# Kernel tuning notes

Measured on AMD Instinct MI355X. Metric: run time of the kernel, lower is better.

## Reference

```python
import jax, jax.numpy as jnp
import numpy as np

B, T, C = 2, 2048, 1024
NUM_HEADS, QK_LEN, V_LEN = 16, 64, 64


def setup_inputs() -> dict:
    key = jax.random.key(0)
    ks = jax.random.split(key, 11)
    s = 0.02
    return {
        "Q": jax.random.normal(ks[0], (B, T, C), jnp.float32),
        "K": jax.random.normal(ks[1], (B, T, C), jnp.float32),
        "V": jax.random.normal(ks[2], (B, T, C), jnp.float32),
        # Linear weights stored as (in, out); y = x @ W + b
        "Wq": jax.random.normal(ks[3], (C, NUM_HEADS * QK_LEN), jnp.float32) * s,
        "bq": jnp.zeros((NUM_HEADS * QK_LEN,), jnp.float32),
        "Wk": jax.random.normal(ks[4], (C, NUM_HEADS * QK_LEN), jnp.float32) * s,
        "bk": jnp.zeros((NUM_HEADS * QK_LEN,), jnp.float32),
        "Wv": jax.random.normal(ks[5], (C, NUM_HEADS * V_LEN), jnp.float32) * s,
        "bv": jnp.zeros((NUM_HEADS * V_LEN,), jnp.float32),
        "Wo": jax.random.normal(ks[6], (NUM_HEADS * V_LEN, C), jnp.float32) * s,
        "bo": jnp.zeros((C,), jnp.float32),
    }


def _split_heads(x, n_heads, d):
    b, t, _ = x.shape
    return x.reshape(b, t, n_heads, d).transpose(0, 2, 1, 3)  # (B,H,T,d)


def reference(Q, K, V, Wq, bq, Wk, bk, Wv, bv, Wo, bo):
    q = _split_heads(Q @ Wq + bq, NUM_HEADS, QK_LEN)   # (B,H,T,dk)
    k = _split_heads(K @ Wk + bk, NUM_HEADS, QK_LEN)   # (B,H,T,dk)
    v = _split_heads(V @ Wv + bv, NUM_HEADS, V_LEN)    # (B,H,T,dv)

    scale = 1.0 / jnp.sqrt(jnp.asarray(QK_LEN, q.dtype))
    scores = jnp.einsum("bhqd,bhkd->bhqk", q, k) * scale  # (B,H,T,T)
    attn = jax.nn.softmax(scores, axis=-1)
    out = jnp.einsum("bhqk,bhkd->bhqd", attn, v)           # (B,H,T,dv)

    out = out.transpose(0, 2, 1, 3).reshape(Q.shape[0], Q.shape[1], NUM_HEADS * V_LEN)
    return out @ Wo + bo
```

## Files before the change

### kernel.cpp

```cpp
#include <hip/hip_runtime.h>
#include <hip/hip_bf16.h>
#include <math.h>

constexpr int B = 2, T = 2048, C = 1024, H = 16, D = 64;
constexpr int M = B * T;
constexpr float SCALE_L2E = 0.125f * 1.4426950408889634f;

typedef __attribute__((ext_vector_type(8))) short s16x8;
typedef __attribute__((ext_vector_type(4))) short s16x4;
typedef __attribute__((ext_vector_type(4))) float fv4;

typedef unsigned short ushort_t;

static __device__ __forceinline__ ushort_t f2bf(float x) {
    union { float f; unsigned u; } c; c.f = x;
    unsigned u = c.u + 0x7FFFu + ((c.u >> 16) & 1u);
    return (ushort_t)(u >> 16);
}

static __device__ __forceinline__ int cvt_pk_bf16(float lo, float hi) {
    int r;
    asm("v_cvt_pk_bf16_f32 %0, %1, %2" : "=v"(r) : "v"(lo), "v"(hi));
    return r;
}

#define GLDS(gp, lp) __builtin_amdgcn_global_load_lds( \
    (const __attribute__((address_space(1))) void*)(gp), \
    (__attribute__((address_space(3))) void*)(lp), 16, 0, 0)

__global__ __launch_bounds__(256) void prep(
    const float* __restrict__ W0, const float* __restrict__ W1,
    const float* __restrict__ W2, const float* __restrict__ W3,
    ushort_t* __restrict__ Wt)
{
    __shared__ ushort_t tile[64][72];
    const int tid = threadIdx.x;
    const int idx = blockIdx.x;
    const int s = idx >> 8;
    const float* W = (s == 0) ? W0 : (s == 1) ? W1 : (s == 2) ? W2 : W3;
    const int k0 = (idx & 15) * 64, n0 = ((idx >> 4) & 15) * 64;
#pragma unroll
    for (int it = 0; it < 4; it++) {
        int f = it * 256 + tid;
        int r = f >> 4, c4 = (f & 15) * 4;
        float4 x = *(const float4*)(W + (size_t)(k0 + r) * C + n0 + c4);
        *(int*)&tile[r][c4]     = cvt_pk_bf16(x.x, x.y);
        *(int*)&tile[r][c4 + 2] = cvt_pk_bf16(x.z, x.w);
    }
    __syncthreads();
#pragma unroll
    for (int it = 0; it < 4; it++) {
        int f = it * 256 + tid;
        int rr = f >> 4, c4 = (f & 15) * 4;
        union { s16x4 v; ushort_t u[4]; } u;
#pragma unroll
        for (int j = 0; j < 4; j++) u.u[j] = tile[c4 + j][rr];
        *(s16x4*)(Wt + (size_t)(s * 1024 + n0 + rr) * 1024 + k0 + c4) = u.v;
    }
}

__global__ __launch_bounds__(256) void gemm_qkv(
    const float* __restrict__ Qf, const float* __restrict__ Kf,
    const float* __restrict__ Vf, const ushort_t* __restrict__ Wt,
    const float* __restrict__ bq, const float* __restrict__ bk,
    const float* __restrict__ bv,
    ushort_t* __restrict__ qw, ushort_t* __restrict__ kw,
    ushort_t* __restrict__ vt)
{
    __shared__ ushort_t sm[17408];
    ushort_t* As0 = sm;
    ushort_t* Bs0 = sm + 8192;

    const int tid = threadIdx.x;
    const int w = tid >> 6, lane = tid & 63;
    const int quad = lane >> 4, lc = lane & 15;
    const int wm = w & 1, wn = w >> 1;

    const int lin = blockIdx.y * 24 + blockIdx.x;
    const int xcd = lin % 8;
    const int i_ = lin / 8;
    const int s = i_ >> 5;
    const int r_ = i_ & 31;
    const int m0 = (xcd * 4 + (r_ >> 3)) * 128;
    const int nt = s * 8 + (r_ & 7);
    const int nsec0 = (nt & 7) * 128;

    const float* Af = (s == 0) ? Qf : (s == 1) ? Kf : Vf;
    const ushort_t* Btbase = Wt + (size_t)nt * 128 * 1024;

    const int srow = (w << 4) + (lane >> 2);
    const int ske  = (lane & 3) * 8;

    const int ar = tid >> 1;
    const int ah = (tid & 1) * 16;
    const float* apb = Af + (size_t)(m0 + ar) * 1024 + ah;

    fv4 acc[4][4] = {};

    auto stageB = [&](int k0, int buf) {
#pragma unroll
        for (int i = 0; i < 2; i++) {
            int row = i * 64 + srow;
            GLDS(Btbase + (size_t)row * 1024 + k0 + ske,
                 Bs0 + buf * 4096 + i * 2048 + w * 512);
        }
    };
    float4 areg[4];
    auto loadA = [&](int k0) {
        const float4* p = (const float4*)(apb + k0);
        areg[0] = p[0]; areg[1] = p[1]; areg[2] = p[2]; areg[3] = p[3];
    };
    auto writeA = [&](int buf) {
        union { s16x8 v; int i[4]; } u0, u1;
        u0.i[0] = cvt_pk_bf16(areg[0].x, areg[0].y);
        u0.i[1] = cvt_pk_bf16(areg[0].z, areg[0].w);
        u0.i[2] = cvt_pk_bf16(areg[1].x, areg[1].y);
        u0.i[3] = cvt_pk_bf16(areg[1].z, areg[1].w);
        u1.i[0] = cvt_pk_bf16(areg[2].x, areg[2].y);
        u1.i[1] = cvt_pk_bf16(areg[2].z, areg[2].w);
        u1.i[2] = cvt_pk_bf16(areg[3].x, areg[3].y);
        u1.i[3] = cvt_pk_bf16(areg[3].z, areg[3].w);
        ushort_t* dst = As0 + buf * 4096 + ar * 32 + ah;
        *(s16x8*)dst = u0.v;
        *(s16x8*)(dst + 8) = u1.v;
    };

    stageB(0, 0);
    loadA(0);
    writeA(0);
    __syncthreads();

    for (int k0 = 0; k0 < 1024; k0 += 32) {
        const int cur = (k0 >> 5) & 1;
        const bool pf = (k0 + 32 < 1024);
        if (pf) { stageB(k0 + 32, cur ^ 1); loadA(k0 + 32); }

        s16x8 af[4], bf[4];
#pragma unroll
        for (int ms = 0; ms < 4; ms++)
            af[ms] = *(const s16x8*)(As0 + cur * 4096 + (wm * 64 + ms * 16 + lc) * 32 + quad * 8);
#pragma unroll
        for (int ns = 0; ns < 4; ns++)
            bf[ns] = *(const s16x8*)(Bs0 + cur * 4096 + (wn * 64 + ns * 16 + lc) * 32 + quad * 8);
#pragma unroll
        for (int ms = 0; ms < 4; ms++)
#pragma unroll
            for (int ns = 0; ns < 4; ns++)
                acc[ms][ns] = __builtin_amdgcn_mfma_f32_16x16x32_bf16(
                    af[ms], bf[ns], acc[ms][ns], 0, 0, 0);

        if (pf) writeA(cur ^ 1);
        __syncthreads();
    }

    if (s == 2) {
        ushort_t* tp = sm;
#pragma unroll
        for (int ns = 0; ns < 4; ns++) {
            const int nl = wn * 64 + ns * 16 + lc;
            const float bias = bv[nsec0 + nl];
#pragma unroll
            for (int ms = 0; ms < 4; ms++) {
                const int ml = wm * 64 + ms * 16 + quad * 4;
                union { s16x4 v; int i2[2]; } u;
                u.i2[0] = cvt_pk_bf16(acc[ms][ns][0] + bias, acc[ms][ns][1] + bias);
                u.i2[1] = cvt_pk_bf16(acc[ms][ns][2] + bias, acc[ms][ns][3] + bias);
                *(s16x4*)&tp[nl * 136 + ml] = u.v;
            }
        }
        __syncthreads();
        const int b_ = m0 >> 11, t0 = m0 & 2047;
#pragma unroll
        for (int it = 0; it < 8; it++) {
            const int row = it * 16 + (tid >> 4);
            const int ch = tid & 15;
            const int n = nsec0 + row;
            const int h_ = n >> 6, d_ = n & 63;
            s16x8 v8 = *(const s16x8*)&tp[row * 136 + ch * 8];
            *(s16x8*)(vt + ((size_t)(b_ * H + h_) * 64 + d_) * T + t0 + ch * 8) = v8;
        }
        return;
    }

    const float* biasp = (s == 0) ? bq : bk;
    const float premul = (s == 0) ? SCALE_L2E : 1.0f;
    ushort_t* outp = (s == 0) ? qw : kw;

#pragma unroll
    for (int ns = 0; ns < 4; ns++) {
        const int nl = nsec0 + wn * 64 + ns * 16 + lc;
        const float bias = biasp[nl];
        const int h_ = nl >> 6, d_ = nl & 63;
#pragma unroll
        for (int ms = 0; ms < 4; ms++) {
#pragma unroll
            for (int r = 0; r < 4; r++) {
                int m = m0 + wm * 64 + ms * 16 + quad * 4 + r;
                float val = (acc[ms][ns][r] + bias) * premul;
                int b_ = m >> 11, t_ = m & (T - 1);
                size_t bh = (size_t)(b_ * H + h_);
                outp[((bh * T + t_) << 6) + d_] = f2bf(val);
            }
        }
    }
}

__global__ __launch_bounds__(256) void gemm_final(
    const ushort_t* __restrict__ A, const ushort_t* __restrict__ Wot,
    const float* __restrict__ bo, float* __restrict__ out)
{
    __shared__ ushort_t As[2][128 * 32];
    __shared__ ushort_t Bs[2][64 * 32];

    const int tid = threadIdx.x;
    const int w = tid >> 6, lane = tid & 63;
    const int quad = lane >> 4, lc = lane & 15;
    const int wm = w & 1, wn = w >> 1;

    const int lin = blockIdx.y * 16 + blockIdx.x;
    const int xcd = lin & 7;
    const int i_ = lin >> 3;
    const int m0 = (xcd * 4 + (i_ >> 4)) * 128;
    const int n0 = (i_ & 15) * 64;

    const int srow = (w << 4) + (lane >> 2);
    const int ske  = (lane & 3) * 8;

    fv4 acc[4][2] = {};

    auto stage = [&](int k0, int buf) {
        GLDS(A + (size_t)(m0 + srow) * 1024 + k0 + ske,      As[buf] + w * 512);
        GLDS(A + (size_t)(m0 + 64 + srow) * 1024 + k0 + ske, As[buf] + 2048 + w * 512);
        GLDS(Wot + (size_t)(n0 + srow) * 1024 + k0 + ske,    Bs[buf] + w * 512);
    };

    stage(0, 0);
    __syncthreads();

    for (int k0 = 0; k0 < 1024; k0 += 32) {
        const int cur = (k0 >> 5) & 1;
        if (k0 + 32 < 1024) stage(k0 + 32, cur ^ 1);

        s16x8 af[4], bf[2];
#pragma unroll
        for (int ms = 0; ms < 4; ms++)
            af[ms] = *(const s16x8*)(As[cur] + (wm * 64 + ms * 16 + lc) * 32 + quad * 8);
#pragma unroll
        for (int ns = 0; ns < 2; ns++)
            bf[ns] = *(const s16x8*)(Bs[cur] + (wn * 32 + ns * 16 + lc) * 32 + quad * 8);
#pragma unroll
        for (int ms = 0; ms < 4; ms++)
#pragma unroll
            for (int ns = 0; ns < 2; ns++)
                acc[ms][ns] = __builtin_amdgcn_mfma_f32_16x16x32_bf16(
                    af[ms], bf[ns], acc[ms][ns], 0, 0, 0);
        __syncthreads();
    }

#pragma unroll
    for (int ns = 0; ns < 2; ns++) {
        const int n = n0 + wn * 32 + ns * 16 + lc;
        const float bias = bo[n];
#pragma unroll
        for (int ms = 0; ms < 4; ms++) {
#pragma unroll
            for (int r = 0; r < 4; r++) {
                int m = m0 + wm * 64 + ms * 16 + quad * 4 + r;
                out[(size_t)m * 1024 + n] = acc[ms][ns][r] + bias;
            }
        }
    }
}

__global__ __launch_bounds__(256, 4) void attn(
    const ushort_t* __restrict__ q, const ushort_t* __restrict__ k,
    const ushort_t* __restrict__ vT, ushort_t* __restrict__ o)
{
    __shared__ alignas(16) ushort_t ks[2][64 * 64];
    __shared__ alignas(16) ushort_t vs[2][64 * 64];

    const int tid = threadIdx.x;
    const int w = tid >> 6, lane = tid & 63;
    const int quad = lane >> 4, lc = lane & 15;
    const int cs = lc & 7;
    const int qsub = w & 1, ksub = w >> 1;

    const int id = blockIdx.y * 32 + blockIdx.x;
    const int qt = (id >> 3) & 31;
    const int bh = (id & 7) * 4 + (id >> 8);

    s16x8 aq[2][2];
    const ushort_t* qb = q + ((size_t)bh * T + qt * 64 + qsub * 32) * D;
#pragma unroll
    for (int j = 0; j < 2; j++)
#pragma unroll
        for (int h = 0; h < 2; h++)
            aq[j][h] = *(const s16x8*)(qb + (size_t)(j * 16 + lc) * D + h * 32 + quad * 8);

    fv4 accO[2][4] = {};
    float psum[2] = {0.f, 0.f};

    const ushort_t* kb0 = k + (size_t)bh * T * D;
    const ushort_t* vb0 = vT + (size_t)bh * D * T;

    const int sr8 = lane >> 3;
    const int sch = (lane & 7) ^ sr8;

    auto stage = [&](int kt, int buf) {
#pragma unroll
        for (int i = 0; i < 2; i++) {
            const int r = w * 16 + i * 8 + sr8;
            GLDS(kb0 + (size_t)(kt * 64 + r) * 64 + sch * 8,
                 ks[buf] + (w * 16 + i * 8) * 64);
            GLDS(vb0 + (size_t)r * T + kt * 64 + sch * 8,
                 vs[buf] + (w * 16 + i * 8) * 64);
        }
    };

    stage(0, 0);
    __syncthreads();

    for (int kt = 0; kt < T / 64; kt++) {
        const int cur = kt & 1;
        if (kt + 1 < T / 64) stage(kt + 1, cur ^ 1);

        fv4 accST[2][2] = {};
        __builtin_amdgcn_s_setprio(1);
#pragma unroll
        for (int t4k = 0; t4k < 2; t4k++) {
            const int row = ksub * 32 + t4k * 16 + lc;
            s16x8 ak0 = *(const s16x8*)(ks[cur] + row * 64 + ((quad ^ cs) << 3));
            s16x8 ak1 = *(const s16x8*)(ks[cur] + row * 64 + (((quad + 4) ^ cs) << 3));
#pragma unroll
            for (int j = 0; j < 2; j++) {
                accST[j][t4k] = __builtin_amdgcn_mfma_f32_16x16x32_bf16(
                    ak0, aq[j][0], accST[j][t4k], 0, 0, 0);
                accST[j][t4k] = __builtin_amdgcn_mfma_f32_16x16x32_bf16(
                    ak1, aq[j][1], accST[j][t4k], 0, 0, 0);
            }
        }
        __builtin_amdgcn_s_setprio(0);

        s16x8 av[4];
#pragma unroll
        for (int t4v = 0; t4v < 4; t4v++) {
            const int row = t4v * 16 + lc;
            av[t4v] = *(const s16x8*)(vs[cur] + row * 64 + (((ksub * 4 + quad) ^ cs) << 3));
        }

#pragma unroll
        for (int j = 0; j < 2; j++) {
            float p0 = __builtin_amdgcn_exp2f(accST[j][0][0]);
            float p1 = __builtin_amdgcn_exp2f(accST[j][0][1]);
            float p2 = __builtin_amdgcn_exp2f(accST[j][0][2]);
            float p3 = __builtin_amdgcn_exp2f(accST[j][0][3]);
            float p4 = __builtin_amdgcn_exp2f(accST[j][1][0]);
            float p5 = __builtin_amdgcn_exp2f(accST[j][1][1]);
            float p6 = __builtin_amdgcn_exp2f(accST[j][1][2]);
            float p7 = __builtin_amdgcn_exp2f(accST[j][1][3]);
            psum[j] += ((p0 + p1) + (p2 + p3)) + ((p4 + p5) + (p6 + p7));

            int W00 = cvt_pk_bf16(p0, p1);
            int W01 = cvt_pk_bf16(p2, p3);
            int W10 = cvt_pk_bf16(p4, p5);
            int W11 = cvt_pk_bf16(p6, p7);
            asm("v_permlane32_swap_b32 %0, %1" : "+v"(W00), "+v"(W10));
            asm("v_permlane16_swap_b32 %0, %1" : "+v"(W00), "+v"(W10));
            asm("v_permlane32_swap_b32 %0, %1" : "+v"(W01), "+v"(W11));
            asm("v_permlane16_swap_b32 %0, %1" : "+v"(W01), "+v"(W11));

            union { int i[4]; s16x8 v; } pbu;
            pbu.i[0] = W00; pbu.i[1] = W01; pbu.i[2] = W10; pbu.i[3] = W11;

            __builtin_amdgcn_s_setprio(1);
#pragma unroll
            for (int t4v = 0; t4v < 4; t4v++)
                accO[j][t4v] = __builtin_amdgcn_mfma_f32_16x16x32_bf16(
                    av[t4v], pbu.v, accO[j][t4v], 0, 0, 0);
            __builtin_amdgcn_s_setprio(0);
        }

        __syncthreads();
    }

#pragma unroll
    for (int j = 0; j < 2; j++) {
        psum[j] += __shfl_xor(psum[j], 16);
        psum[j] += __shfl_xor(psum[j], 32);
    }

    float* sc = (float*)&ks[0][0];
#pragma unroll
    for (int c = 0; c < 4; c++) {
        const int j = c >> 1, tv = (c & 1) * 2;
        __syncthreads();
        if (ksub == 1) {
            *(fv4*)(sc + ((qsub * 64 + lane) * 8))     = accO[j][tv];
            *(fv4*)(sc + ((qsub * 64 + lane) * 8 + 4)) = accO[j][tv + 1];
        }
        __syncthreads();
        if (ksub == 0) {
            accO[j][tv]     += *(fv4*)(sc + ((qsub * 64 + lane) * 8));
            accO[j][tv + 1] += *(fv4*)(sc + ((qsub * 64 + lane) * 8 + 4));
        }
    }
    __syncthreads();
    if (ksub == 1) {
        sc[(qsub * 64 + lane) * 2]     = psum[0];
        sc[(qsub * 64 + lane) * 2 + 1] = psum[1];
    }
    __syncthreads();
    if (ksub == 0) {
        psum[0] += sc[(qsub * 64 + lane) * 2];
        psum[1] += sc[(qsub * 64 + lane) * 2 + 1];

        const int b_ = bh >> 4, h_ = bh & 15;
#pragma unroll
        for (int j = 0; j < 2; j++) {
            float inv = 1.0f / psum[j];
            int row = qt * 64 + qsub * 32 + j * 16 + lc;
            ushort_t* op = o + ((size_t)b_ * T + row) * C + h_ * 64;
#pragma unroll
            for (int t4v = 0; t4v < 4; t4v++) {
                union { s16x4 v; int i[2]; } u;
                u.i[0] = cvt_pk_bf16(accO[j][t4v][0] * inv, accO[j][t4v][1] * inv);
                u.i[1] = cvt_pk_bf16(accO[j][t4v][2] * inv, accO[j][t4v][3] * inv);
                *(s16x4*)(op + t4v * 16 + quad * 4) = u.v;
            }
        }
    }
}

extern "C" void kernel_launch(void* const* d_in, const int* in_sizes, int n_in,
                              void* d_out, int out_size, void* d_ws, size_t ws_size,
                              hipStream_t stream)
{
    const float* Q  = (const float*)d_in[0];
    const float* K  = (const float*)d_in[1];
    const float* V  = (const float*)d_in[2];
    const float* Wq = (const float*)d_in[3];
    const float* bq = (const float*)d_in[4];
    const float* Wk = (const float*)d_in[5];
    const float* bk = (const float*)d_in[6];
    const float* Wv = (const float*)d_in[7];
    const float* bv = (const float*)d_in[8];
    const float* Wo = (const float*)d_in[9];
    const float* bo = (const float*)d_in[10];
    float* out = (float*)d_out;

    ushort_t* ow = (ushort_t*)d_ws;
    ushort_t* Wt = ow + (size_t)3 * M * C;
    ushort_t* qw = Wt + (size_t)4096 * 1024;
    ushort_t* kw = qw + (size_t)M * C;
    ushort_t* vt = kw + (size_t)M * C;
    ushort_t* Wot = Wt + (size_t)3072 * 1024;

    dim3 blk(256);
    prep<<<dim3(1024), blk, 0, stream>>>(Wq, Wk, Wv, Wo, Wt);
    gemm_qkv<<<dim3(24, 32), blk, 0, stream>>>(Q, K, V, Wt, bq, bk, bv, qw, kw, vt);
    attn<<<dim3(T / 64, B * H), blk, 0, stream>>>(qw, kw, vt, ow);
    gemm_final<<<dim3(16, 32), blk, 0, stream>>>(ow, Wot, bo, out);
}
```

Baseline: 262.7 us.

## Prefetch fp32 A tile two stages ahead and remap A load lanes

Changes the QKV GEMM's activation staging so each thread loads fp32 A rows using a lane-to-row mapping that matches the B staging pattern. Global loads for A are issued two k-steps ahead, and the bf16 conversion plus LDS write happens at the start of the iteration instead of after the MFMAs. The aim is to hide more global-load latency behind compute, at the cost of holding the prefetched A registers across an extra stage.

Result: faster. 253.4 us (-3.5%).

```diff
diff --git a/kernel.cpp b/kernel.cpp
--- a/kernel.cpp
+++ b/kernel.cpp
@@ -67,7 +67,7 @@
     ushort_t* __restrict__ qw, ushort_t* __restrict__ kw,
     ushort_t* __restrict__ vt)
 {
-    __shared__ ushort_t sm[17408];
+    __shared__ alignas(16) ushort_t sm[17408];
     ushort_t* As0 = sm;
     ushort_t* Bs0 = sm + 8192;
 
@@ -91,11 +91,13 @@
     const int srow = (w << 4) + (lane >> 2);
     const int ske  = (lane & 3) * 8;
 
-    const int ar = tid >> 1;
-    const int ah = (tid & 1) * 16;
-    const float* apb = Af + (size_t)(m0 + ar) * 1024 + ah;
+    const int ar0 = (w << 5) + (lane >> 2);
+    const int ach = (lane & 3) * 8;
+    const float* apb0 = Af + (size_t)(m0 + ar0) * 1024 + ach;
+    const float* apb1 = apb0 + (size_t)16 * 1024;
 
     fv4 acc[4][4] = {};
+    float4 ra[4];
 
     auto stageB = [&](int k0, int buf) {
 #pragma unroll
@@ -105,35 +107,40 @@
                  Bs0 + buf * 4096 + i * 2048 + w * 512);
         }
     };
-    float4 areg[4];
     auto loadA = [&](int k0) {
-        const float4* p = (const float4*)(apb + k0);
-        areg[0] = p[0]; areg[1] = p[1]; areg[2] = p[2]; areg[3] = p[3];
+        ra[0] = *(const float4*)(apb0 + k0);
+        ra[1] = *(const float4*)(apb0 + k0 + 4);
+        ra[2] = *(const float4*)(apb1 + k0);
+        ra[3] = *(const float4*)(apb1 + k0 + 4);
     };
     auto writeA = [&](int buf) {
         union { s16x8 v; int i[4]; } u0, u1;
-        u0.i[0] = cvt_pk_bf16(areg[0].x, areg[0].y);
-        u0.i[1] = cvt_pk_bf16(areg[0].z, areg[0].w);
-        u0.i[2] = cvt_pk_bf16(areg[1].x, areg[1].y);
-        u0.i[3] = cvt_pk_bf16(areg[1].z, areg[1].w);
-        u1.i[0] = cvt_pk_bf16(areg[2].x, areg[2].y);
-        u1.i[1] = cvt_pk_bf16(areg[2].z, areg[2].w);
-        u1.i[2] = cvt_pk_bf16(areg[3].x, areg[3].y);
-        u1.i[3] = cvt_pk_bf16(areg[3].z, areg[3].w);
-        ushort_t* dst = As0 + buf * 4096 + ar * 32 + ah;
-        *(s16x8*)dst = u0.v;
-        *(s16x8*)(dst + 8) = u1.v;
+        u0.i[0] = cvt_pk_bf16(ra[0].x, ra[0].y);
+        u0.i[1] = cvt_pk_bf16(ra[0].z, ra[0].w);
+        u0.i[2] = cvt_pk_bf16(ra[1].x, ra[1].y);
+        u0.i[3] = cvt_pk_bf16(ra[1].z, ra[1].w);
+        u1.i[0] = cvt_pk_bf16(ra[2].x, ra[2].y);
+        u1.i[1] = cvt_pk_bf16(ra[2].z, ra[2].w);
+        u1.i[2] = cvt_pk_bf16(ra[3].x, ra[3].y);
+        u1.i[3] = cvt_pk_bf16(ra[3].z, ra[3].w);
+        *(s16x8*)(As0 + buf * 4096 + ar0 * 32 + ach) = u0.v;
+        *(s16x8*)(As0 + buf * 4096 + (ar0 + 16) * 32 + ach) = u1.v;
     };
 
+    loadA(0);
     stageB(0, 0);
-    loadA(0);
     writeA(0);
+    loadA(32);
     __syncthreads();
 
     for (int k0 = 0; k0 < 1024; k0 += 32) {
         const int cur = (k0 >> 5) & 1;
         const bool pf = (k0 + 32 < 1024);
-        if (pf) { stageB(k0 + 32, cur ^ 1); loadA(k0 + 32); }
+        if (pf) {
+            writeA(cur ^ 1);
+            stageB(k0 + 32, cur ^ 1);
+        }
+        if (k0 + 64 < 1024) loadA(k0 + 64);
 
         s16x8 af[4], bf[4];
 #pragma unroll
@@ -148,8 +155,6 @@
             for (int ns = 0; ns < 4; ns++)
                 acc[ms][ns] = __builtin_amdgcn_mfma_f32_16x16x32_bf16(
                     af[ms], bf[ns], acc[ms][ns], 0, 0, 0);
-
-        if (pf) writeA(cur ^ 1);
         __syncthreads();
     }
 
```
